# Kernel tuning notes

Hardware: AMD Instinct MI355X
Metric: run time of the kernel (lower is better)

Reference implementation:

```python
import jax, jax.numpy as jnp
import numpy as np

NUM_NODES = 500000
EMB = 200        # embedding_size
U = 32           # embedding_u_size
T = 4            # edge_type_count
DIM_A = 32
B = 16384        # batch of training pairs
NN = 10          # sampled neighbors per edge type


def setup_inputs() -> dict:
    key = jax.random.key(0)
    ks = jax.random.split(key, 8)
    inv_sqrt_e = 1.0 / np.sqrt(EMB).astype(np.float32)
    return {
        "train_inputs": jax.random.randint(ks[0], (B,), 0, NUM_NODES, dtype=jnp.int32),
        "train_types": jax.random.randint(ks[1], (B,), 0, T, dtype=jnp.int32),
        "node_neigh": jax.random.randint(ks[2], (B, T, NN), 0, NUM_NODES, dtype=jnp.int32),
        # learned parameters (init matches reset_parameters)
        "node_embeddings": jax.random.uniform(ks[3], (NUM_NODES, EMB), minval=-1.0, maxval=1.0, dtype=jnp.float32),
        "node_type_embeddings": jax.random.uniform(ks[4], (NUM_NODES, T, U), minval=-1.0, maxval=1.0, dtype=jnp.float32),
        "trans_weights": jax.random.normal(ks[5], (T, U, EMB), dtype=jnp.float32) * inv_sqrt_e,
        "trans_weights_s1": jax.random.normal(ks[6], (T, U, DIM_A), dtype=jnp.float32) * inv_sqrt_e,
        "trans_weights_s2": jax.random.normal(ks[7], (T, DIM_A, 1), dtype=jnp.float32) * inv_sqrt_e,
    }


def reference(train_inputs, train_types, node_neigh,
              node_embeddings, node_type_embeddings,
              trans_weights, trans_weights_s1, trans_weights_s2):
    # Per-edge-type neighbor aggregation (copy_src + sum in the DGL code):
    # for layer l: sum_n node_type_embeddings[node_neigh[b, l, n], l, :]
    layer_idx = jnp.arange(T, dtype=node_neigh.dtype)[None, :, None]      # [1,T,1]
    neigh = node_type_embeddings[node_neigh, layer_idx, :]                # [B,T,NN,U] gather
    node_type_embed = neigh.sum(axis=2)                                   # [B,T,U]

    tw  = trans_weights[train_types]                                      # [B,U,EMB]
    tw1 = trans_weights_s1[train_types]                                   # [B,U,A]
    tw2 = trans_weights_s2[train_types][..., 0]                           # [B,A]

    # attention over edge types
    h = jnp.tanh(jnp.einsum('btu,bua->bta', node_type_embed, tw1))        # [B,T,A]
    scores = jnp.einsum('bta,ba->bt', h, tw2)                             # [B,T]
    att = jax.nn.softmax(scores, axis=1)                                  # [B,T]
    comb = jnp.einsum('bt,btu->bu', att, node_type_embed)                 # [B,U]

    node_embed = node_embeddings[train_inputs] + jnp.einsum('bu,bue->be', comb, tw)  # [B,EMB]
    norm = jnp.maximum(jnp.linalg.norm(node_embed, axis=1, keepdims=True), 1e-12)
    return node_embed / norm
```

## Files before the change

kernel.cpp:

```cpp
#include <hip/hip_runtime.h>

#define EMB 200
#define U_DIM 32
#define T_DIM 4
#define DIM_A 32
#define NN 10
#define BLK 1024
#define NWAVE 16
#define BPW 4
#define TW_FLOATS (T_DIM * U_DIM * EMB)

__global__ __launch_bounds__(BLK, 4) void gatne_fused(
    const int* __restrict__ train_inputs,
    const int* __restrict__ train_types,
    const int* __restrict__ node_neigh,
    const float* __restrict__ node_emb,
    const float* __restrict__ node_type_emb,
    const float* __restrict__ tw,
    const float* __restrict__ tw1,
    const float* __restrict__ tw2,
    float* __restrict__ out)
{
    __shared__ float s_tw[TW_FLOATS];
    __shared__ float s_nte[NWAVE][T_DIM][U_DIM];
    __shared__ float s_comb[NWAVE][U_DIM];

    const int wid  = threadIdx.x >> 6;
    const int lane = threadIdx.x & 63;
    const int u    = lane & 31;
    const int th   = lane >> 5;
    const int base = blockIdx.x * (NWAVE * BPW);

    int nb[BPW], ty[BPW], nd[BPW];
    #pragma unroll
    for (int i = 0; i < BPW; ++i) {
        const int b = base + i * NWAVE + wid;
        nb[i] = (lane < T_DIM * NN) ? node_neigh[b * T_DIM * NN + lane] : 0;
        ty[i] = train_types[b];
        nd[i] = train_inputs[b];
    }

    {
        const float4* src = (const float4*)tw;
        float4*       dst = (float4*)s_tw;
        #pragma unroll
        for (int k = 0; k < 7; ++k) {
            const int i = threadIdx.x + k * BLK;
            if (i < TW_FLOATS / 4) dst[i] = src[i];
        }
    }

    float g[2][2][NN];

    #pragma unroll
    for (int tt = 0; tt < 2; ++tt) {
        const int t = tt * 2 + th;
        #pragma unroll
        for (int n = 0; n < NN; ++n) {
            const int idx = __shfl(nb[0], t * NN + n, 64);
            g[0][tt][n] = node_type_emb[((long)idx * T_DIM + t) * U_DIM + u];
        }
    }

    float4 nv_cur = make_float4(0.f, 0.f, 0.f, 0.f);
    if (lane < EMB / 4)
        nv_cur = *(const float4*)(node_emb + (size_t)nd[0] * EMB + lane * 4);

    __syncthreads();

    #pragma unroll
    for (int i = 0; i < BPW; ++i) {
        const int cb   = i & 1;
        const int nbuf = cb ^ 1;
        const int b    = base + i * NWAVE + wid;
        const int type = ty[i];

        #pragma unroll
        for (int tt = 0; tt < 2; ++tt) {
            const int t = tt * 2 + th;
            float a0 = 0.f;
            #pragma unroll
            for (int n = 0; n < NN; ++n) a0 += g[cb][tt][n];
            s_nte[wid][t][u] = a0;
        }

        if (i + 1 < BPW) {
            #pragma unroll
            for (int tt = 0; tt < 2; ++tt) {
                const int t = tt * 2 + th;
                #pragma unroll
                for (int n = 0; n < NN; ++n) {
                    const int idx = __shfl(nb[i + 1], t * NN + n, 64);
                    g[nbuf][tt][n] = node_type_emb[((long)idx * T_DIM + t) * U_DIM + u];
                }
            }
        }

        float4 nv_next = make_float4(0.f, 0.f, 0.f, 0.f);
        if (i + 1 < BPW && lane < EMB / 4)
            nv_next = *(const float4*)(node_emb + (size_t)nd[i + 1] * EMB + lane * 4);

        const float* tw1p = tw1 + type * U_DIM * DIM_A;
        const float  w2   = tw2[type * DIM_A + u];
        float sc[2];
        #pragma unroll
        for (int tt = 0; tt < 2; ++tt) {
            const int t = tt * 2 + th;
            float a1 = 0.f;
            #pragma unroll
            for (int uu = 0; uu < U_DIM; ++uu)
                a1 += s_nte[wid][t][uu] * tw1p[uu * DIM_A + u];
            float s = tanhf(a1) * w2;
            #pragma unroll
            for (int m = 1; m < 32; m <<= 1) s += __shfl_xor(s, m, 64);
            sc[tt] = s;
        }
        const float o0 = __shfl_xor(sc[0], 32, 64);
        const float o1 = __shfl_xor(sc[1], 32, 64);
        const float s0 = th ? o0    : sc[0];
        const float s1 = th ? sc[0] : o0;
        const float s2 = th ? o1    : sc[1];
        const float s3 = th ? sc[1] : o1;

        const float mx  = fmaxf(fmaxf(s0, s1), fmaxf(s2, s3));
        const float e0  = __expf(s0 - mx), e1 = __expf(s1 - mx);
        const float e2  = __expf(s2 - mx), e3 = __expf(s3 - mx);
        const float inv = 1.f / (e0 + e1 + e2 + e3);
        const float comb = (e0 * s_nte[wid][0][u] + e1 * s_nte[wid][1][u] +
                            e2 * s_nte[wid][2][u] + e3 * s_nte[wid][3][u]) * inv;
        if (lane < 32) s_comb[wid][u] = comb;

        const float* twp = s_tw + type * U_DIM * EMB;
        float4 v = nv_cur;
        if (lane < EMB / 4) {
            #pragma unroll 8
            for (int uu = 0; uu < U_DIM; ++uu) {
                const float  cg = s_comb[wid][uu];
                const float4 w  = *(const float4*)(twp + uu * EMB + lane * 4);
                v.x += cg * w.x; v.y += cg * w.y; v.z += cg * w.z; v.w += cg * w.w;
            }
        }
        float ss = (lane < EMB / 4) ? (v.x * v.x + v.y * v.y + v.z * v.z + v.w * v.w) : 0.f;
        #pragma unroll
        for (int m = 1; m < 64; m <<= 1) ss += __shfl_xor(ss, m, 64);
        const float rinv = 1.f / fmaxf(sqrtf(ss), 1e-12f);
        if (lane < EMB / 4) {
            float4 o = make_float4(v.x * rinv, v.y * rinv, v.z * rinv, v.w * rinv);
            *(float4*)(out + (size_t)b * EMB + lane * 4) = o;
        }
        nv_cur = nv_next;
    }
}

extern "C" void kernel_launch(void* const* d_in, const int* in_sizes, int n_in,
                              void* d_out, int out_size, void* d_ws, size_t ws_size,
                              hipStream_t stream) {
    const int*   train_inputs = (const int*)d_in[0];
    const int*   train_types  = (const int*)d_in[1];
    const int*   node_neigh   = (const int*)d_in[2];
    const float* node_emb     = (const float*)d_in[3];
    const float* node_type_e  = (const float*)d_in[4];
    const float* tw           = (const float*)d_in[5];
    const float* tw1          = (const float*)d_in[6];
    const float* tw2          = (const float*)d_in[7];
    float*       out          = (float*)d_out;

    const int B = in_sizes[0];
    const int blocks = B / (NWAVE * BPW);

    gatne_fused<<<blocks, BLK, 0, stream>>>(
        train_inputs, train_types, node_neigh,
        node_emb, node_type_e, tw, tw1, tw2, out);
}
```

Before: 40.23 us.

## Drop shared trans_weights staging; group batch rows by type for register reuse

Result: slower. 89.73 us (+123.1%).

```diff
diff --git a/kernel.cpp b/kernel.cpp
--- a/kernel.cpp
+++ b/kernel.cpp
@@ -5,12 +5,12 @@
 #define T_DIM 4
 #define DIM_A 32
 #define NN 10
-#define BLK 1024
-#define NWAVE 16
+#define NWAVE 4
 #define BPW 4
-#define TW_FLOATS (T_DIM * U_DIM * EMB)
-
-__global__ __launch_bounds__(BLK, 4) void gatne_fused(
+#define NB (NWAVE * BPW)
+#define G 4
+
+__global__ __launch_bounds__(256, 4) void gatne(
     const int* __restrict__ train_inputs,
     const int* __restrict__ train_types,
     const int* __restrict__ node_neigh,
@@ -21,84 +21,71 @@
     const float* __restrict__ tw2,
     float* __restrict__ out)
 {
-    __shared__ float s_tw[TW_FLOATS];
-    __shared__ float s_nte[NWAVE][T_DIM][U_DIM];
-    __shared__ float s_comb[NWAVE][U_DIM];
-
-    const int wid  = threadIdx.x >> 6;
-    const int lane = threadIdx.x & 63;
+    __shared__ __align__(16) float s_nte[NWAVE][T_DIM][U_DIM];
+    __shared__ __align__(16) float s_comb[NB][U_DIM];
+    __shared__ int s_list[T_DIM][NB];
+    __shared__ int s_node[NB];
+    __shared__ int s_cnt[T_DIM];
+
+    const int tid  = threadIdx.x;
+    const int wid  = tid >> 6;
+    const int lane = tid & 63;
     const int u    = lane & 31;
     const int th   = lane >> 5;
-    const int base = blockIdx.x * (NWAVE * BPW);
-
-    int nb[BPW], ty[BPW], nd[BPW];
+    const int base = blockIdx.x * NB;
+
+    if (tid < T_DIM) s_cnt[tid] = 0;
+
+    int nb[BPW], ty[BPW];
     #pragma unroll
     for (int i = 0; i < BPW; ++i) {
         const int b = base + i * NWAVE + wid;
         nb[i] = (lane < T_DIM * NN) ? node_neigh[b * T_DIM * NN + lane] : 0;
         ty[i] = train_types[b];
-        nd[i] = train_inputs[b];
-    }
-
-    {
-        const float4* src = (const float4*)tw;
-        float4*       dst = (float4*)s_tw;
-        #pragma unroll
-        for (int k = 0; k < 7; ++k) {
-            const int i = threadIdx.x + k * BLK;
-            if (i < TW_FLOATS / 4) dst[i] = src[i];
-        }
     }
 
     float g[2][2][NN];
-
     #pragma unroll
     for (int tt = 0; tt < 2; ++tt) {
-        const int t = tt * 2 + th;
         #pragma unroll
         for (int n = 0; n < NN; ++n) {
-            const int idx = __shfl(nb[0], t * NN + n, 64);
-            g[0][tt][n] = node_type_emb[((long)idx * T_DIM + t) * U_DIM + u];
-        }
-    }
-
-    float4 nv_cur = make_float4(0.f, 0.f, 0.f, 0.f);
-    if (lane < EMB / 4)
-        nv_cur = *(const float4*)(node_emb + (size_t)nd[0] * EMB + lane * 4);
-
+            const int i0 = __builtin_amdgcn_readlane(nb[0], (2 * tt) * NN + n);
+            const int i1 = __builtin_amdgcn_readlane(nb[0], (2 * tt + 1) * NN + n);
+            const int idx = th ? i1 : i0;
+            g[0][tt][n] = node_type_emb[((long)idx * T_DIM + (2 * tt + th)) * U_DIM + u];
+        }
+    }
     __syncthreads();
 
     #pragma unroll
     for (int i = 0; i < BPW; ++i) {
-        const int cb   = i & 1;
-        const int nbuf = cb ^ 1;
-        const int b    = base + i * NWAVE + wid;
+        const int cb = i & 1, nx = cb ^ 1;
+        const int b  = base + i * NWAVE + wid;
+        const int lb = i * NWAVE + wid;
         const int type = ty[i];
 
         #pragma unroll
         for (int tt = 0; tt < 2; ++tt) {
-            const int t = tt * 2 + th;
-            float a0 = 0.f;
-            #pragma unroll
-            for (int n = 0; n < NN; ++n) a0 += g[cb][tt][n];
-            s_nte[wid][t][u] = a0;
+            float a = 0.f;
+            #pragma unroll
+            for (int n = 0; n < NN; ++n) a += g[cb][tt][n];
+            s_nte[wid][tt * 2 + th][u] = a;
         }
 
         if (i + 1 < BPW) {
             #pragma unroll
             for (int tt = 0; tt < 2; ++tt) {
-                const int t = tt * 2 + th;
                 #pragma unroll
                 for (int n = 0; n < NN; ++n) {
-                    const int idx = __shfl(nb[i + 1], t * NN + n, 64);
-                    g[nbuf][tt][n] = node_type_emb[((long)idx * T_DIM + t) * U_DIM + u];
+                    const int i0 = __builtin_amdgcn_readlane(nb[i + 1], (2 * tt) * NN + n);
+                    const int i1 = __builtin_amdgcn_readlane(nb[i + 1], (2 * tt + 1) * NN + n);
+                    const int idx = th ? i1 : i0;
+                    g[nx][tt][n] = node_type_emb[((long)idx * T_DIM + (2 * tt + th)) * U_DIM + u];
                 }
             }
         }
 
-        float4 nv_next = make_float4(0.f, 0.f, 0.f, 0.f);
-        if (i + 1 < BPW && lane < EMB / 4)
-            nv_next = *(const float4*)(node_emb + (size_t)nd[i + 1] * EMB + lane * 4);
+        const int ndv = train_inputs[b];
 
         const float* tw1p = tw1 + type * U_DIM * DIM_A;
         const float  w2   = tw2[type * DIM_A + u];
@@ -108,8 +95,13 @@
             const int t = tt * 2 + th;
             float a1 = 0.f;
             #pragma unroll
-            for (int uu = 0; uu < U_DIM; ++uu)
-                a1 += s_nte[wid][t][uu] * tw1p[uu * DIM_A + u];
+            for (int q = 0; q < 8; ++q) {
+                const float4 bc = *(const float4*)&s_nte[wid][t][q * 4];
+                a1 += bc.x * tw1p[(q * 4 + 0) * DIM_A + u];
+                a1 += bc.y * tw1p[(q * 4 + 1) * DIM_A + u];
+                a1 += bc.z * tw1p[(q * 4 + 2) * DIM_A + u];
+                a1 += bc.w * tw1p[(q * 4 + 3) * DIM_A + u];
+            }
             float s = tanhf(a1) * w2;
             #pragma unroll
             for (int m = 1; m < 32; m <<= 1) s += __shfl_xor(s, m, 64);
@@ -128,27 +120,80 @@
         const float inv = 1.f / (e0 + e1 + e2 + e3);
         const float comb = (e0 * s_nte[wid][0][u] + e1 * s_nte[wid][1][u] +
                             e2 * s_nte[wid][2][u] + e3 * s_nte[wid][3][u]) * inv;
-        if (lane < 32) s_comb[wid][u] = comb;
-
-        const float* twp = s_tw + type * U_DIM * EMB;
-        float4 v = nv_cur;
-        if (lane < EMB / 4) {
-            #pragma unroll 8
-            for (int uu = 0; uu < U_DIM; ++uu) {
-                const float  cg = s_comb[wid][uu];
-                const float4 w  = *(const float4*)(twp + uu * EMB + lane * 4);
-                v.x += cg * w.x; v.y += cg * w.y; v.z += cg * w.z; v.w += cg * w.w;
-            }
-        }
-        float ss = (lane < EMB / 4) ? (v.x * v.x + v.y * v.y + v.z * v.z + v.w * v.w) : 0.f;
-        #pragma unroll
-        for (int m = 1; m < 64; m <<= 1) ss += __shfl_xor(ss, m, 64);
-        const float rinv = 1.f / fmaxf(sqrtf(ss), 1e-12f);
-        if (lane < EMB / 4) {
-            float4 o = make_float4(v.x * rinv, v.y * rinv, v.z * rinv, v.w * rinv);
-            *(float4*)(out + (size_t)b * EMB + lane * 4) = o;
-        }
-        nv_cur = nv_next;
+        if (lane < 32) s_comb[lb][u] = comb;
+        if (lane == 0) {
+            s_node[lb] = ndv;
+            const int sl = atomicAdd(&s_cnt[type], 1);
+            s_list[type][sl] = lb;
+        }
+    }
+    __syncthreads();
+
+    const int  c   = lane;
+    const int  cc  = (c < EMB / 4 - 1) ? c : (EMB / 4 - 1);
+    const bool act = c < EMB / 4;
+
+    const int c0 = s_cnt[0], c1 = s_cnt[1], c2 = s_cnt[2], c3 = s_cnt[3];
+    const int p0 = (c0 + G - 1) / G;
+    const int p1 = p0 + (c1 + G - 1) / G;
+    const int p2 = p1 + (c2 + G - 1) / G;
+    const int gtot = p2 + (c3 + G - 1) / G;
+
+    for (int gi = wid; gi < gtot; gi += NWAVE) {
+        int t, off, cnt_t;
+        if      (gi < p0) { t = 0; off = gi;      cnt_t = c0; }
+        else if (gi < p1) { t = 1; off = gi - p0; cnt_t = c1; }
+        else if (gi < p2) { t = 2; off = gi - p1; cnt_t = c2; }
+        else              { t = 3; off = gi - p2; cnt_t = c3; }
+        const int cb2 = off * G;
+        const int n   = min(G, cnt_t - cb2);
+
+        const int bsel = min((lane >> 3) & 3, n - 1);
+        const int lbs  = s_list[t][cb2 + bsel];
+        const float4 cr4 = *(const float4*)&s_comb[lbs][(lane & 7) * 4];
+        const float crf[4] = {cr4.x, cr4.y, cr4.z, cr4.w};
+
+        int lbk[G];
+        #pragma unroll
+        for (int k = 0; k < G; ++k) lbk[k] = s_list[t][cb2 + min(k, n - 1)];
+
+        float4 nv[G];
+        #pragma unroll
+        for (int k = 0; k < G; ++k) {
+            const int nd = s_node[lbk[k]];
+            nv[k] = *(const float4*)(node_emb + (size_t)nd * EMB + cc * 4);
+        }
+
+        float4 acc[G];
+        #pragma unroll
+        for (int k = 0; k < G; ++k) acc[k] = make_float4(0.f, 0.f, 0.f, 0.f);
+
+        const float* twp = tw + (size_t)t * U_DIM * EMB + cc * 4;
+        #pragma unroll
+        for (int uu = 0; uu < U_DIM; ++uu) {
+            const float4 wv = *(const float4*)(twp + uu * EMB);
+            #pragma unroll
+            for (int k = 0; k < G; ++k) {
+                const float cg = __int_as_float(__builtin_amdgcn_readlane(
+                    __float_as_int(crf[uu & 3]), k * 8 + (uu >> 2)));
+                acc[k].x += cg * wv.x; acc[k].y += cg * wv.y;
+                acc[k].z += cg * wv.z; acc[k].w += cg * wv.w;
+            }
+        }
+
+        #pragma unroll
+        for (int k = 0; k < G; ++k) {
+            const float vx = acc[k].x + nv[k].x, vy = acc[k].y + nv[k].y;
+            const float vz = acc[k].z + nv[k].z, vw = acc[k].w + nv[k].w;
+            float ss = act ? (vx * vx + vy * vy + vz * vz + vw * vw) : 0.f;
+            #pragma unroll
+            for (int m = 1; m < 64; m <<= 1) ss += __shfl_xor(ss, m, 64);
+            const float rinv = 1.f / fmaxf(sqrtf(ss), 1e-12f);
+            if (act && k < n) {
+                float4 o = make_float4(vx * rinv, vy * rinv, vz * rinv, vw * rinv);
+                *(float4*)(out + (size_t)(base + lbk[k]) * EMB + c * 4) = o;
+            }
+        }
     }
 }
 
@@ -166,9 +211,9 @@
     float*       out          = (float*)d_out;
 
     const int B = in_sizes[0];
-    const int blocks = B / (NWAVE * BPW);
-
-    gatne_fused<<<blocks, BLK, 0, stream>>>(
+    const int blocks = B / NB;
+
+    gatne<<<blocks, NWAVE * 64, 0, stream>>>(
         train_inputs, train_types, node_neigh,
         node_emb, node_type_e, tw, tw1, tw2, out);
 }
```

## Halve block size, double rows per wave, use readlane for broadcasts

Applied to the files above, without the earlier changes.

Result: faster. 35.84 us (-10.9%).

```diff
diff --git a/kernel.cpp b/kernel.cpp
--- a/kernel.cpp
+++ b/kernel.cpp
@@ -5,12 +5,16 @@
 #define T_DIM 4
 #define DIM_A 32
 #define NN 10
-#define BLK 1024
-#define NWAVE 16
-#define BPW 4
+#define BLK 512
+#define NWAVE 8
+#define BPW 8
 #define TW_FLOATS (T_DIM * U_DIM * EMB)
 
-__global__ __launch_bounds__(BLK, 4) void gatne_fused(
+__device__ __forceinline__ float readlane_f(float v, int l) {
+    return __int_as_float(__builtin_amdgcn_readlane(__float_as_int(v), l));
+}
+
+__global__ __launch_bounds__(BLK, 2) void gatne_fused(
     const int* __restrict__ train_inputs,
     const int* __restrict__ train_types,
     const int* __restrict__ node_neigh,
@@ -22,8 +26,7 @@
     float* __restrict__ out)
 {
     __shared__ float s_tw[TW_FLOATS];
-    __shared__ float s_nte[NWAVE][T_DIM][U_DIM];
-    __shared__ float s_comb[NWAVE][U_DIM];
+    __shared__ __align__(16) float s_nte[NWAVE][T_DIM][U_DIM];
 
     const int wid  = threadIdx.x >> 6;
     const int lane = threadIdx.x & 63;
@@ -44,21 +47,21 @@
         const float4* src = (const float4*)tw;
         float4*       dst = (float4*)s_tw;
         #pragma unroll
-        for (int k = 0; k < 7; ++k) {
+        for (int k = 0; k < 13; ++k) {
             const int i = threadIdx.x + k * BLK;
             if (i < TW_FLOATS / 4) dst[i] = src[i];
         }
     }
 
     float g[2][2][NN];
-
     #pragma unroll
     for (int tt = 0; tt < 2; ++tt) {
-        const int t = tt * 2 + th;
         #pragma unroll
         for (int n = 0; n < NN; ++n) {
-            const int idx = __shfl(nb[0], t * NN + n, 64);
-            g[0][tt][n] = node_type_emb[((long)idx * T_DIM + t) * U_DIM + u];
+            const int i0 = __builtin_amdgcn_readlane(nb[0], (2 * tt) * NN + n);
+            const int i1 = __builtin_amdgcn_readlane(nb[0], (2 * tt + 1) * NN + n);
+            const int idx = th ? i1 : i0;
+            g[0][tt][n] = node_type_emb[((long)idx * T_DIM + (2 * tt + th)) * U_DIM + u];
         }
     }
 
@@ -71,27 +74,27 @@
     #pragma unroll
     for (int i = 0; i < BPW; ++i) {
         const int cb   = i & 1;
-        const int nbuf = cb ^ 1;
+        const int nx   = cb ^ 1;
         const int b    = base + i * NWAVE + wid;
         const int type = ty[i];
 
         #pragma unroll
         for (int tt = 0; tt < 2; ++tt) {
-            const int t = tt * 2 + th;
             float a0 = 0.f;
             #pragma unroll
             for (int n = 0; n < NN; ++n) a0 += g[cb][tt][n];
-            s_nte[wid][t][u] = a0;
+            s_nte[wid][tt * 2 + th][u] = a0;
         }
 
         if (i + 1 < BPW) {
             #pragma unroll
             for (int tt = 0; tt < 2; ++tt) {
-                const int t = tt * 2 + th;
                 #pragma unroll
                 for (int n = 0; n < NN; ++n) {
-                    const int idx = __shfl(nb[i + 1], t * NN + n, 64);
-                    g[nbuf][tt][n] = node_type_emb[((long)idx * T_DIM + t) * U_DIM + u];
+                    const int i0 = __builtin_amdgcn_readlane(nb[i + 1], (2 * tt) * NN + n);
+                    const int i1 = __builtin_amdgcn_readlane(nb[i + 1], (2 * tt + 1) * NN + n);
+                    const int idx = th ? i1 : i0;
+                    g[nx][tt][n] = node_type_emb[((long)idx * T_DIM + (2 * tt + th)) * U_DIM + u];
                 }
             }
         }
@@ -108,8 +111,13 @@
             const int t = tt * 2 + th;
             float a1 = 0.f;
             #pragma unroll
-            for (int uu = 0; uu < U_DIM; ++uu)
-                a1 += s_nte[wid][t][uu] * tw1p[uu * DIM_A + u];
+            for (int q = 0; q < 8; ++q) {
+                const float4 bc = *(const float4*)&s_nte[wid][t][q * 4];
+                a1 += bc.x * tw1p[(q * 4 + 0) * DIM_A + u];
+                a1 += bc.y * tw1p[(q * 4 + 1) * DIM_A + u];
+                a1 += bc.z * tw1p[(q * 4 + 2) * DIM_A + u];
+                a1 += bc.w * tw1p[(q * 4 + 3) * DIM_A + u];
+            }
             float s = tanhf(a1) * w2;
             #pragma unroll
             for (int m = 1; m < 32; m <<= 1) s += __shfl_xor(s, m, 64);
@@ -128,14 +136,13 @@
         const float inv = 1.f / (e0 + e1 + e2 + e3);
         const float comb = (e0 * s_nte[wid][0][u] + e1 * s_nte[wid][1][u] +
                             e2 * s_nte[wid][2][u] + e3 * s_nte[wid][3][u]) * inv;
-        if (lane < 32) s_comb[wid][u] = comb;
 
         const float* twp = s_tw + type * U_DIM * EMB;
         float4 v = nv_cur;
         if (lane < EMB / 4) {
-            #pragma unroll 8
+            #pragma unroll
             for (int uu = 0; uu < U_DIM; ++uu) {
-                const float  cg = s_comb[wid][uu];
+                const float  cg = readlane_f(comb, uu);
                 const float4 w  = *(const float4*)(twp + uu * EMB + lane * 4);
                 v.x += cg * w.x; v.y += cg * w.y; v.z += cg * w.z; v.w += cg * w.w;
             }
```
